# Performance work log

Measured on AMD Instinct MI355X. Metric: run time of the kernel, lower is better.

The kernel has to match this reference:

```python
import jax, jax.numpy as jnp
import numpy as np

DIM = 1024
DIM_HEADS = 128   # dim_inner
HEADS = 8         # dim_out // dim_heads
DHEAD = DIM_HEADS // HEADS  # = 16, per the Rearrange '(qkv h d)'
EPS = 1e-6


def setup_inputs() -> dict:
    key = jax.random.key(0)
    k1, k2, k3 = jax.random.split(key, 3)
    x = jax.random.normal(k1, (8, 4096, DIM), dtype=jnp.float32)
    norm_weight = jnp.ones((DIM,), dtype=jnp.float32)
    w_qkv = jax.random.normal(k2, (3 * DIM_HEADS, DIM), dtype=jnp.float32) * (1.0 / np.sqrt(DIM))
    temperature = jnp.zeros((HEADS, 1, 1), dtype=jnp.float32)
    w_out = jax.random.normal(k3, (DIM, DIM_HEADS), dtype=jnp.float32) * (1.0 / np.sqrt(DIM_HEADS))
    return {"x": x, "norm_weight": norm_weight, "w_qkv": w_qkv,
            "temperature": temperature, "w_out": w_out}


def _l2norm(t, axis=-1):
    # F.normalize(p=2): divide by max(||t||, eps) with eps=1e-12
    n = jnp.sqrt(jnp.sum(t * t, axis=axis, keepdims=True))
    return t / jnp.maximum(n, 1e-12)


def reference(x, norm_weight, w_qkv, temperature, w_out):
    b, n, _ = x.shape
    # RMSNorm
    ms = jnp.mean(x * x, axis=-1, keepdims=True)
    xn = x * jax.lax.rsqrt(ms + EPS) * norm_weight
    # QKV projection: b n (3 h d) -> 3 b h d n
    qkv = jnp.einsum('bnc,oc->bno', xn, w_qkv)
    qkv = qkv.reshape(b, n, 3, HEADS, DHEAD).transpose(2, 0, 3, 4, 1)  # [3,b,h,d,n]
    q, k, v = qkv[0], qkv[1], qkv[2]
    # l2-normalize along token axis (last axis, n)
    q = _l2norm(q)
    k = _l2norm(k)
    q = q * jnp.exp(temperature)  # (h,1,1) broadcasts over (b,h,d,n)
    # XCiT channel (cross-covariance) attention: d x d similarity over tokens
    sim = jnp.einsum('bhin,bhjn->bhij', q, k)
    attn = jax.nn.softmax(sim, axis=-1)
    out = jnp.einsum('bhij,bhjn->bhin', attn, v)  # [b,h,d,n]
    # b h d n -> b n (h d), then output projection
    out = out.transpose(0, 3, 1, 2).reshape(b, n, HEADS * DHEAD)
    return jnp.einsum('bnc,oc->bno', out, w_out)
```

## Files before the change

kernel.cpp:

```cpp
#include <hip/hip_runtime.h>
#include <hip/hip_bf16.h>
#include <stdint.h>

typedef __bf16 bf16_t;
typedef __bf16 bf16x8 __attribute__((ext_vector_type(8)));
typedef float  f32x4  __attribute__((ext_vector_type(4)));

#define DIM    1024
#define NTOK   4096
#define NB     8
#define ROWS   (NB*NTOK)
#define QKVC   384
#define INNER  128

#define GLD16(g, l) __builtin_amdgcn_global_load_lds( \
    (const __attribute__((address_space(1))) void*)(g), \
    (__attribute__((address_space(3))) void*)(l), 16, 0, 0)

#define VMCNT(n) asm volatile("s_waitcnt vmcnt(" #n ")" ::: "memory")
#define SBAR0()  __builtin_amdgcn_sched_barrier(0)

#define OFF_WQ    131072u
#define OFF_QKV   1048576u
#define OFF_STATS 26214400u
#define OFF_ATTN  30932992u
#define OFF_WEFF  30998528u

__global__ __launch_bounds__(256) void k_wconv(const float* __restrict__ wq,
    const float* __restrict__ nw, bf16_t* __restrict__ wqb)
{
    int o = blockIdx.x;
    int c = threadIdx.x * 4;
    float4 wv = *reinterpret_cast<const float4*>(wq + (size_t)o*DIM + c);
    float4 nv = *reinterpret_cast<const float4*>(nw + c);
    bf16_t* dst = wqb + (size_t)o*DIM + c;
    dst[0]=(bf16_t)(wv.x*nv.x); dst[1]=(bf16_t)(wv.y*nv.y);
    dst[2]=(bf16_t)(wv.z*nv.z); dst[3]=(bf16_t)(wv.w*nv.w);
}

__global__ __launch_bounds__(512, 2) void k_qkv_gemm(const float* __restrict__ x,
    const bf16_t* __restrict__ wqb, bf16_t* __restrict__ qkv,
    float* __restrict__ stats)
{
    __shared__ bf16_t Al[2][128*64];
    __shared__ bf16_t Bl[2][384*64];
    __shared__ float srow[128];
    int mt = blockIdx.x;
    int row0 = mt*128;
    int t = threadIdx.x;
    int lane = t & 63, lr = lane & 15, lg = lane >> 4;
    int w = t >> 6, wm = w >> 2, wn = w & 3;

    int rA = t >> 2;
    int fo = (t & 3) * 16;
    const float* xrow = x + (size_t)(row0 + rA)*DIM + fo;
    int ws0 = ((t & 3)*2)     ^ (rA & 7);
    int ws1 = ((t & 3)*2 + 1) ^ (rA & 7);

    int srB = t >> 3;
    int sk8 = ((t & 7) ^ (srB & 7)) * 8;
    const bf16_t* bbase = wqb + (size_t)srB*DIM + sk8;
    int ldsoff = (t & ~63) * 8;

    int rsw = lr & 7;

    float4 sa0, sa1, sa2, sa3;
    float4 sb0, sb1, sb2, sb3;

#define LOADA_(r0, r1, r2, r3, kt) do {                                  \
        const float4* _xs = reinterpret_cast<const float4*>(xrow + (kt)*64); \
        r0 = _xs[0]; r1 = _xs[1]; r2 = _xs[2]; r3 = _xs[3];              \
    } while (0)

#define STAGEB(buf, kt) do {                                             \
        int _ko = (kt)*64;                                               \
        _Pragma("unroll")                                                \
        for (int _c = 0; _c < 6; _c++)                                   \
            GLD16(bbase + _ko + (size_t)(64*_c)*DIM,                     \
                  &Bl[buf][ldsoff + _c*4096]);                           \
    } while (0)

#define WRITEA_(r0, r1, r2, r3, buf) do {                                \
        ssq += r0.x*r0.x + r0.y*r0.y + r0.z*r0.z + r0.w*r0.w             \
             + r1.x*r1.x + r1.y*r1.y + r1.z*r1.z + r1.w*r1.w             \
             + r2.x*r2.x + r2.y*r2.y + r2.z*r2.z + r2.w*r2.w             \
             + r3.x*r3.x + r3.y*r3.y + r3.z*r3.z + r3.w*r3.w;            \
        bf16x8 _v0, _v1;                                                 \
        _v0[0]=(bf16_t)r0.x; _v0[1]=(bf16_t)r0.y; _v0[2]=(bf16_t)r0.z;   \
        _v0[3]=(bf16_t)r0.w; _v0[4]=(bf16_t)r1.x; _v0[5]=(bf16_t)r1.y;   \
        _v0[6]=(bf16_t)r1.z; _v0[7]=(bf16_t)r1.w;                        \
        _v1[0]=(bf16_t)r2.x; _v1[1]=(bf16_t)r2.y; _v1[2]=(bf16_t)r2.z;   \
        _v1[3]=(bf16_t)r2.w; _v1[4]=(bf16_t)r3.x; _v1[5]=(bf16_t)r3.y;   \
        _v1[6]=(bf16_t)r3.z; _v1[7]=(bf16_t)r3.w;                        \
        *reinterpret_cast<bf16x8*>(&Al[buf][rA*64 + ws0*8]) = _v0;       \
        *reinterpret_cast<bf16x8*>(&Al[buf][rA*64 + ws1*8]) = _v1;       \
    } while (0)

#define COMPUTE(CUR) do {                                                \
        _Pragma("unroll")                                                \
        for (int kk = 0; kk < 2; kk++) {                                 \
            int kb = ((kk*4 + lg) ^ rsw) * 8;                            \
            bf16x8 af[4], bfr[6];                                        \
            _Pragma("unroll")                                            \
            for (int mi = 0; mi < 4; mi++)                               \
                af[mi] = *reinterpret_cast<const bf16x8*>(               \
                    &Al[CUR][(wm*64 + mi*16 + lr)*64 + kb]);             \
            _Pragma("unroll")                                            \
            for (int ni = 0; ni < 6; ni++)                               \
                bfr[ni] = *reinterpret_cast<const bf16x8*>(              \
                    &Bl[CUR][(wn*96 + ni*16 + lr)*64 + kb]);             \
            _Pragma("unroll")                                            \
            for (int mi = 0; mi < 4; mi++)                               \
                _Pragma("unroll")                                        \
                for (int ni = 0; ni < 6; ni++)                           \
                    acc[mi][ni] = __builtin_amdgcn_mfma_f32_16x16x32_bf16( \
                        af[mi], bfr[ni], acc[mi][ni], 0, 0, 0);          \
        }                                                                \
    } while (0)

#define STEP(kt, CUR, L0, L1, L2, L3, W0, W1, W2, W3) do {               \
        if ((kt) + 1 < 16) STAGEB((CUR)^1, (kt)+1);                      \
        SBAR0();                                                         \
        if ((kt) + 2 < 16) LOADA_(L0, L1, L2, L3, (kt)+2);               \
        SBAR0();                                                         \
        COMPUTE(CUR);                                                    \
        if ((kt) + 1 < 16) {                                             \
            WRITEA_(W0, W1, W2, W3, (CUR)^1);     \
            if ((kt) + 2 < 16) VMCNT(4); else VMCNT(0);                  \
            SBAR0();                                                     \
            asm volatile("s_waitcnt lgkmcnt(0)" ::: "memory");           \
        }                                                                \
        __builtin_amdgcn_s_barrier();                                    \
    } while (0)

    float ssq = 0.f;
    f32x4 acc[4][6] = {};

    STAGEB(0, 0);
    SBAR0();
    LOADA_(sa0, sa1, sa2, sa3, 0);
    LOADA_(sb0, sb1, sb2, sb3, 1);
    SBAR0();
    WRITEA_(sa0, sa1, sa2, sa3, 0);
    asm volatile("s_waitcnt lgkmcnt(0)" ::: "memory");
    __builtin_amdgcn_s_barrier();

    for (int kt2 = 0; kt2 < 16; kt2 += 2) {
        STEP(kt2,     0, sa0, sa1, sa2, sa3, sb0, sb1, sb2, sb3);
        STEP(kt2 + 1, 1, sb0, sb1, sb2, sb3, sa0, sa1, sa2, sa3);
    }
#undef LOADA_
#undef STAGEB
#undef WRITEA_
#undef COMPUTE
#undef STEP

    ssq += __shfl_xor(ssq, 1, 64);
    ssq += __shfl_xor(ssq, 2, 64);
    if ((t & 3) == 0) srow[rA] = rsqrtf(ssq*(1.0f/DIM) + 1e-6f);
    __syncthreads();

    bf16_t* qk = &Bl[0][0];
    #pragma unroll
    for (int mi = 0; mi < 4; mi++)
        #pragma unroll
        for (int ni = 0; ni < 6; ni++) {
            int col_g = wn*96 + ni*16 + lr;
            #pragma unroll
            for (int rr = 0; rr < 4; rr++) {
                int rloc = wm*64 + mi*16 + lg*4 + rr;
                bf16_t val = (bf16_t)(acc[mi][ni][rr] * srow[rloc]);
                if (wn*96 + ni*16 >= 256)
                    qkv[(size_t)(row0 + rloc)*QKVC + col_g] = val;
                else
                    qk[rloc*256 + col_g] = val;
            }
        }
    __syncthreads();

    {
        int h = w;
        f32x4 g = {};
        #pragma unroll
        for (int ks = 0; ks < 4; ks++) {
            bf16x8 afr, bfr2;
            #pragma unroll
            for (int e = 0; e < 8; e++) {
                int tt = ks*32 + lg*8 + e;
                afr[e]  = qk[tt*256 + h*16 + lr];
                bfr2[e] = qk[tt*256 + 128 + h*16 + lr];
            }
            g = __builtin_amdgcn_mfma_f32_16x16x32_bf16(afr, bfr2, g, 0, 0, 0);
        }
        float* base = stats + ((size_t)mt*8 + h)*288;
        #pragma unroll
        for (int reg = 0; reg < 4; reg++)
            base[(lg*4 + reg)*16 + lr] = g[reg];
        float qs = 0.f, ks2 = 0.f;
        #pragma unroll
        for (int e = 0; e < 32; e++) {
            int tt = lg*32 + e;
            float qv = (float)qk[tt*256 + h*16 + lr];
            float kv = (float)qk[tt*256 + 128 + h*16 + lr];
            qs += qv*qv; ks2 += kv*kv;
        }
        qs  += __shfl_xor(qs, 16, 64);  qs  += __shfl_xor(qs, 32, 64);
        ks2 += __shfl_xor(ks2, 16, 64); ks2 += __shfl_xor(ks2, 32, 64);
        if (lane < 16) { base[256 + lr] = qs; base[272 + lr] = ks2; }
    }
}

__global__ __launch_bounds__(256) void k_attn(const float* __restrict__ stats,
    const float* __restrict__ temp, float* __restrict__ attn)
{
    int bid = blockIdx.x;
    int b = bid >> 3, h = bid & 7;
    int t = threadIdx.x, i = t >> 4, j = t & 15;
    float gsum = 0.f, qs = 0.f, ks = 0.f;
    for (int ch = 0; ch < 32; ch++) {
        const float* base = stats + ((size_t)(b*32 + ch)*8 + h)*288;
        gsum += base[i*16 + j];
        qs   += base[256 + i];
        ks   += base[272 + j];
    }
    float et  = expf(temp[h]);
    float sim = gsum * et / (fmaxf(sqrtf(qs), 1e-12f) * fmaxf(sqrtf(ks), 1e-12f));
    float m = sim;
    #pragma unroll
    for (int d = 1; d < 16; d <<= 1) m = fmaxf(m, __shfl_xor(m, d, 16));
    float e = expf(sim - m);
    float ssum = e;
    #pragma unroll
    for (int d = 1; d < 16; d <<= 1) ssum += __shfl_xor(ssum, d, 16);
    attn[((size_t)(b*8 + h)*16 + i)*16 + j] = e / ssum;
}

__global__ __launch_bounds__(256) void k_weff(const float* __restrict__ attn,
    const float* __restrict__ wout, bf16_t* __restrict__ weff)
{
    __shared__ float at[2048];
    int bid = blockIdx.x;
    int b = bid >> 5, ob = (bid & 31)*32;
    int t = threadIdx.x;
    #pragma unroll
    for (int r = 0; r < 8; r++) at[t + 256*r] = attn[(size_t)b*2048 + t + 256*r];
    __syncthreads();
    int c = t & 127, h = c >> 4, j = c & 15, oo = (t >> 7)*16;
    #pragma unroll
    for (int m = 0; m < 16; m++) {
        int o = ob + oo + m;
        float acc = 0.f;
        #pragma unroll
        for (int i2 = 0; i2 < 16; i2++)
            acc += wout[(size_t)o*INNER + h*16 + i2] * at[(h*16 + i2)*16 + j];
        weff[((size_t)b*DIM + o)*INNER + c] = (bf16_t)acc;
    }
}

__global__ __launch_bounds__(256) void k_out_gemm(const bf16_t* __restrict__ qkv,
    const bf16_t* __restrict__ weff, float* __restrict__ out)
{
    __shared__ bf16_t Al[128*136];
    __shared__ bf16_t Bl[128*136];
    int bid = blockIdx.x;
    int b = bid >> 8, rem = bid & 255;
    int mt = rem >> 3, nt = rem & 7;
    int tok0 = mt*128, o0 = nt*128;
    int t = threadIdx.x;
    #pragma unroll
    for (int rd = 0; rd < 8; rd++) {
        int r  = (t >> 4) + 16*rd;
        int c8 = (t & 15) * 8;
        *reinterpret_cast<uint4*>(&Al[r*136 + c8]) =
            *reinterpret_cast<const uint4*>(
                qkv + ((size_t)b*NTOK + tok0 + r)*QKVC + 256 + c8);
        *reinterpret_cast<uint4*>(&Bl[r*136 + c8]) =
            *reinterpret_cast<const uint4*>(
                weff + ((size_t)b*DIM + o0 + r)*INNER + c8);
    }
    __syncthreads();
    int w = t >> 6, lane = t & 63, lr = lane & 15, lg = lane >> 4;
    int wr = (w & 1)*64, wc = (w >> 1)*64;
    f32x4 acc[4][4] = {};
    #pragma unroll
    for (int kk = 0; kk < 4; kk++) {
        int kb = kk*32 + lg*8;
        bf16x8 af[4], bfr[4];
        #pragma unroll
        for (int mi = 0; mi < 4; mi++)
            af[mi] = *reinterpret_cast<const bf16x8*>(&Al[(wr + mi*16 + lr)*136 + kb]);
        #pragma unroll
        for (int ni = 0; ni < 4; ni++)
            bfr[ni] = *reinterpret_cast<const bf16x8*>(&Bl[(wc + ni*16 + lr)*136 + kb]);
        #pragma unroll
        for (int mi = 0; mi < 4; mi++)
            #pragma unroll
            for (int ni = 0; ni < 4; ni++)
                acc[mi][ni] = __builtin_amdgcn_mfma_f32_16x16x32_bf16(
                    af[mi], bfr[ni], acc[mi][ni], 0, 0, 0);
    }
    #pragma unroll
    for (int mi = 0; mi < 4; mi++)
        #pragma unroll
        for (int ni = 0; ni < 4; ni++) {
            int col_g = o0 + wc + ni*16 + lr;
            #pragma unroll
            for (int r = 0; r < 4; r++) {
                int row_g = tok0 + wr + mi*16 + lg*4 + r;
                out[((size_t)b*NTOK + row_g)*DIM + col_g] = acc[mi][ni][r];
            }
        }
}

extern "C" void kernel_launch(void* const* d_in, const int* in_sizes, int n_in,
                              void* d_out, int out_size, void* d_ws, size_t ws_size,
                              hipStream_t stream)
{
    const float* x    = (const float*)d_in[0];
    const float* nw   = (const float*)d_in[1];
    const float* wq   = (const float*)d_in[2];
    const float* temp = (const float*)d_in[3];
    const float* wout = (const float*)d_in[4];
    float* out = (float*)d_out;

    char* ws = (char*)d_ws;
    bf16_t* wqb   = (bf16_t*)(ws + OFF_WQ);
    bf16_t* qkv   = (bf16_t*)(ws + OFF_QKV);
    float*  stats = (float*)(ws + OFF_STATS);
    float*  attn  = (float*)(ws + OFF_ATTN);
    bf16_t* weff  = (bf16_t*)(ws + OFF_WEFF);

    k_wconv    <<<384,  256, 0, stream>>>(wq, nw, wqb);
    k_qkv_gemm <<<256,  512, 0, stream>>>(x, wqb, qkv, stats);
    k_attn     <<<64,   256, 0, stream>>>(stats, temp, attn);
    k_weff     <<<256,  256, 0, stream>>>(attn, wout, weff);
    k_out_gemm <<<2048, 256, 0, stream>>>(qkv, weff, out);
}
```

Baseline: 102.4 us.

## Single-buffer LDS in QKV GEMM to fit more blocks per CU

Replaces the double-buffered A/B LDS tiles with one shared buffer, which halves LDS use so two 512-thread blocks can share a CU. The launch bound is raised to 4 blocks per CU. The software pipeline is rewritten as a plain per-k-step loop: stage B, write A, prefetch the next A, wait, barrier, compute. This gives up intra-block overlap of loads and MFMA in exchange for more resident waves. The tighter launch bound also caps registers per thread while the accumulator tile alone needs many, so it risks spills.

```diff
diff --git a/kernel.cpp b/kernel.cpp
--- a/kernel.cpp
+++ b/kernel.cpp
@@ -38,13 +38,14 @@
     dst[2]=(bf16_t)(wv.z*nv.z); dst[3]=(bf16_t)(wv.w*nv.w);
 }
 
-__global__ __launch_bounds__(512, 2) void k_qkv_gemm(const float* __restrict__ x,
+__global__ __launch_bounds__(512, 4) void k_qkv_gemm(const float* __restrict__ x,
     const bf16_t* __restrict__ wqb, bf16_t* __restrict__ qkv,
     float* __restrict__ stats)
 {
-    __shared__ bf16_t Al[2][128*64];
-    __shared__ bf16_t Bl[2][384*64];
+    __shared__ bf16_t lds[32768];
     __shared__ float srow[128];
+    bf16_t* Al = lds;
+    bf16_t* Bl = lds + 8192;
     int mt = blockIdx.x;
     int row0 = mt*128;
     int t = threadIdx.x;
@@ -64,39 +65,38 @@
 
     int rsw = lr & 7;
 
-    float4 sa0, sa1, sa2, sa3;
-    float4 sb0, sb1, sb2, sb3;
-
-#define LOADA_(r0, r1, r2, r3, kt) do {                                  \
+    float4 u0, u1, u2, u3;
+
+#define LOADA(kt) do {                                                   \
         const float4* _xs = reinterpret_cast<const float4*>(xrow + (kt)*64); \
-        r0 = _xs[0]; r1 = _xs[1]; r2 = _xs[2]; r3 = _xs[3];              \
+        u0 = _xs[0]; u1 = _xs[1]; u2 = _xs[2]; u3 = _xs[3];              \
     } while (0)
 
-#define STAGEB(buf, kt) do {                                             \
+#define STAGEB(kt) do {                                                  \
         int _ko = (kt)*64;                                               \
         _Pragma("unroll")                                                \
         for (int _c = 0; _c < 6; _c++)                                   \
             GLD16(bbase + _ko + (size_t)(64*_c)*DIM,                     \
-                  &Bl[buf][ldsoff + _c*4096]);                           \
+                  &Bl[ldsoff + _c*4096]);                                \
     } while (0)
 
-#define WRITEA_(r0, r1, r2, r3, buf) do {                                \
-        ssq += r0.x*r0.x + r0.y*r0.y + r0.z*r0.z + r0.w*r0.w             \
-             + r1.x*r1.x + r1.y*r1.y + r1.z*r1.z + r1.w*r1.w             \
-             + r2.x*r2.x + r2.y*r2.y + r2.z*r2.z + r2.w*r2.w             \
-             + r3.x*r3.x + r3.y*r3.y + r3.z*r3.z + r3.w*r3.w;            \
+#define WRITEA() do {                                                   \
+        ssq += u0.x*u0.x + u0.y*u0.y + u0.z*u0.z + u0.w*u0.w             \
+             + u1.x*u1.x + u1.y*u1.y + u1.z*u1.z + u1.w*u1.w             \
+             + u2.x*u2.x + u2.y*u2.y + u2.z*u2.z + u2.w*u2.w             \
+             + u3.x*u3.x + u3.y*u3.y + u3.z*u3.z + u3.w*u3.w;            \
         bf16x8 _v0, _v1;                                                 \
-        _v0[0]=(bf16_t)r0.x; _v0[1]=(bf16_t)r0.y; _v0[2]=(bf16_t)r0.z;   \
-        _v0[3]=(bf16_t)r0.w; _v0[4]=(bf16_t)r1.x; _v0[5]=(bf16_t)r1.y;   \
-        _v0[6]=(bf16_t)r1.z; _v0[7]=(bf16_t)r1.w;                        \
-        _v1[0]=(bf16_t)r2.x; _v1[1]=(bf16_t)r2.y; _v1[2]=(bf16_t)r2.z;   \
-        _v1[3]=(bf16_t)r2.w; _v1[4]=(bf16_t)r3.x; _v1[5]=(bf16_t)r3.y;   \
-        _v1[6]=(bf16_t)r3.z; _v1[7]=(bf16_t)r3.w;                        \
-        *reinterpret_cast<bf16x8*>(&Al[buf][rA*64 + ws0*8]) = _v0;       \
-        *reinterpret_cast<bf16x8*>(&Al[buf][rA*64 + ws1*8]) = _v1;       \
+        _v0[0]=(bf16_t)u0.x; _v0[1]=(bf16_t)u0.y; _v0[2]=(bf16_t)u0.z;   \
+        _v0[3]=(bf16_t)u0.w; _v0[4]=(bf16_t)u1.x; _v0[5]=(bf16_t)u1.y;   \
+        _v0[6]=(bf16_t)u1.z; _v0[7]=(bf16_t)u1.w;                        \
+        _v1[0]=(bf16_t)u2.x; _v1[1]=(bf16_t)u2.y; _v1[2]=(bf16_t)u2.z;   \
+        _v1[3]=(bf16_t)u2.w; _v1[4]=(bf16_t)u3.x; _v1[5]=(bf16_t)u3.y;   \
+        _v1[6]=(bf16_t)u3.z; _v1[7]=(bf16_t)u3.w;                        \
+        *reinterpret_cast<bf16x8*>(&Al[rA*64 + ws0*8]) = _v0;            \
+        *reinterpret_cast<bf16x8*>(&Al[rA*64 + ws1*8]) = _v1;            \
     } while (0)
 
-#define COMPUTE(CUR) do {                                                \
+#define COMPUTE() do {                                                  \
         _Pragma("unroll")                                                \
         for (int kk = 0; kk < 2; kk++) {                                 \
             int kb = ((kk*4 + lg) ^ rsw) * 8;                            \
@@ -104,11 +104,11 @@
             _Pragma("unroll")                                            \
             for (int mi = 0; mi < 4; mi++)                               \
                 af[mi] = *reinterpret_cast<const bf16x8*>(               \
-                    &Al[CUR][(wm*64 + mi*16 + lr)*64 + kb]);             \
+                    &Al[(wm*64 + mi*16 + lr)*64 + kb]);                  \
             _Pragma("unroll")                                            \
             for (int ni = 0; ni < 6; ni++)                               \
                 bfr[ni] = *reinterpret_cast<const bf16x8*>(              \
-                    &Bl[CUR][(wn*96 + ni*16 + lr)*64 + kb]);             \
+                    &Bl[(wn*96 + ni*16 + lr)*64 + kb]);                  \
             _Pragma("unroll")                                            \
             for (int mi = 0; mi < 4; mi++)                               \
                 _Pragma("unroll")                                        \
@@ -118,49 +118,35 @@
         }                                                                \
     } while (0)
 
-#define STEP(kt, CUR, L0, L1, L2, L3, W0, W1, W2, W3) do {               \
-        if ((kt) + 1 < 16) STAGEB((CUR)^1, (kt)+1);                      \
-        SBAR0();                                                         \
-        if ((kt) + 2 < 16) LOADA_(L0, L1, L2, L3, (kt)+2);               \
-        SBAR0();                                                         \
-        COMPUTE(CUR);                                                    \
-        if ((kt) + 1 < 16) {                                             \
-            WRITEA_(W0, W1, W2, W3, (CUR)^1);     \
-            if ((kt) + 2 < 16) VMCNT(4); else VMCNT(0);                  \
-            SBAR0();                                                     \
-            asm volatile("s_waitcnt lgkmcnt(0)" ::: "memory");           \
-        }                                                                \
-        __builtin_amdgcn_s_barrier();                                    \
-    } while (0)
-
     float ssq = 0.f;
     f32x4 acc[4][6] = {};
 
-    STAGEB(0, 0);
-    SBAR0();
-    LOADA_(sa0, sa1, sa2, sa3, 0);
-    LOADA_(sb0, sb1, sb2, sb3, 1);
-    SBAR0();
-    WRITEA_(sa0, sa1, sa2, sa3, 0);
-    asm volatile("s_waitcnt lgkmcnt(0)" ::: "memory");
-    __builtin_amdgcn_s_barrier();
-
-    for (int kt2 = 0; kt2 < 16; kt2 += 2) {
-        STEP(kt2,     0, sa0, sa1, sa2, sa3, sb0, sb1, sb2, sb3);
-        STEP(kt2 + 1, 1, sb0, sb1, sb2, sb3, sa0, sa1, sa2, sa3);
-    }
-#undef LOADA_
+    LOADA(0);
+
+    for (int kt = 0; kt < 16; kt++) {
+        __builtin_amdgcn_s_barrier();
+        STAGEB(kt);
+        SBAR0();
+        WRITEA();
+        SBAR0();
+        if (kt < 15) LOADA(kt + 1);
+        SBAR0();
+        if (kt < 15) VMCNT(2); else VMCNT(0);
+        asm volatile("s_waitcnt lgkmcnt(0)" ::: "memory");
+        __builtin_amdgcn_s_barrier();
+        COMPUTE();
+    }
+#undef LOADA
 #undef STAGEB
-#undef WRITEA_
+#undef WRITEA
 #undef COMPUTE
-#undef STEP
 
     ssq += __shfl_xor(ssq, 1, 64);
     ssq += __shfl_xor(ssq, 2, 64);
     if ((t & 3) == 0) srow[rA] = rsqrtf(ssq*(1.0f/DIM) + 1e-6f);
     __syncthreads();
 
-    bf16_t* qk = &Bl[0][0];
+    bf16_t* qk = lds;
     #pragma unroll
     for (int mi = 0; mi < 4; mi++)
         #pragma unroll
```

Measured after the change: 285.5 us. 2.79x slower.
